# Kernel optimization log

Measured on AMD Instinct MI355X. Metric: run time of the kernel, lower is better.

## Reference

```python
import jax, jax.numpy as jnp
import numpy as np

N = 8192
DIM_IN = 1024
DIM_INNER = 1024
DIM_OUT = 1024


def setup_inputs() -> dict:
    key = jax.random.key(0)
    k1, k2, k3, k4 = jax.random.split(key, 4)
    x = jax.random.normal(k1, (N, DIM_IN), dtype=jnp.float32)
    # torch nn.Linear weights, stored transposed for right-multiplication
    Wqkv = jax.random.normal(k2, (DIM_IN, 3 * DIM_INNER), dtype=jnp.float32) * (DIM_IN ** -0.5)
    Wout = jax.random.normal(k3, (DIM_INNER, DIM_OUT), dtype=jnp.float32) * (DIM_INNER ** -0.5)
    bout = jax.random.normal(k4, (DIM_OUT,), dtype=jnp.float32) * 0.01
    return {"x": x, "Wqkv": Wqkv, "Wout": Wout, "bout": bout}


def reference(x, Wqkv, Wout, bout):
    scale = DIM_INNER ** -0.5
    qkv = x @ Wqkv                      # [N, 3*Di]
    q, k, v = jnp.split(qkv, 3, axis=-1)  # each [N, Di]
    sim = jnp.einsum('id,jd->ij', q, k) * scale  # [N, N]
    # causal mask: future positions (j > i) filled with -finfo.max
    i = jnp.arange(sim.shape[0])[:, None]
    j = jnp.arange(sim.shape[1])[None, :]
    sim = jnp.where(j > i, -jnp.finfo(sim.dtype).max, sim)
    attn = jax.nn.softmax(sim, axis=-1)
    out = jnp.einsum('ij,jd->id', attn, v)  # [N, Di]
    return out @ Wout + bout            # [N, Do]
```

## Files before the change

kernel.cpp:

```cpp
#include <hip/hip_runtime.h>
#include <hip/hip_bf16.h>


typedef __bf16 v8bf __attribute__((ext_vector_type(8)));
typedef float  v4f  __attribute__((ext_vector_type(4)));

struct __align__(8) S4 { short x, y, z, w; };

__device__ inline short f2bf(float f) {
  __hip_bfloat16 h = __float2bfloat16(f);
  return *reinterpret_cast<short*>(&h);
}
__device__ inline float bf2f(short s) {
  unsigned u = ((unsigned)(unsigned short)s) << 16;
  float f;
  __builtin_memcpy(&f, &u, 4);
  return f;
}

__device__ inline void stage_tile(const short* gbase, int ldg, short* lds, int tid) {
#pragma unroll
  for (int p = 0; p < 2; ++p) {
    const int c = p * 256 + tid;
    const int pos = (c & 3) ^ ((c >> 3) & 3);
    const short* g = gbase + (size_t)(c >> 2) * ldg + pos * 8;
    short* l = lds + p * 2048 + (tid >> 6) * 512;
    __builtin_amdgcn_global_load_lds(
        (__attribute__((address_space(1))) void*)(void*)g,
        (__attribute__((address_space(3))) void*)l, 16, 0, 0);
  }
}

__device__ inline void mma_step(const short* As, const short* Bs, v4f acc[4][4],
                                int lane, int wm, int wn) {
  const int qd = lane >> 4, r16 = lane & 15;
  const int sw = (qd ^ ((r16 >> 1) & 3)) * 8;
  const short* ab = As + (wm * 64 + r16) * 32 + sw;
  const short* bb = Bs + (wn * 64 + r16) * 32 + sw;
  v8bf a[4], b[4];
#pragma unroll
  for (int t = 0; t < 4; ++t) {
    a[t] = *(const v8bf*)(ab + t * 512);
    b[t] = *(const v8bf*)(bb + t * 512);
  }
#pragma unroll
  for (int mt = 0; mt < 4; ++mt)
#pragma unroll
    for (int nt = 0; nt < 4; ++nt)
      acc[mt][nt] = __builtin_amdgcn_mfma_f32_16x16x32_bf16(a[mt], b[nt], acc[mt][nt], 0, 0, 0);
}

#define ACC_INIT(acc)                              \
  _Pragma("unroll") for (int i_ = 0; i_ < 4; ++i_) \
  _Pragma("unroll") for (int j_ = 0; j_ < 4; ++j_) \
      acc[i_][j_] = (v4f){0.f, 0.f, 0.f, 0.f};

__global__ __launch_bounds__(256) void k_zerof(float* __restrict__ p, int n) {
  const int i = blockIdx.x * 256 + threadIdx.x;
  if (i < n) p[i] = 0.f;
}

__global__ __launch_bounds__(256) void k_detect(const unsigned short* __restrict__ xs,
                                                int* __restrict__ flag) {
  __shared__ int cnt;
  if (threadIdx.x == 0) cnt = 0;
  __syncthreads();
  int local = 0;
  for (int i = threadIdx.x; i < 4096; i += 256) {
    const unsigned e = (xs[i] >> 7) & 0xFFu;
    if (e >= 0xC0u) ++local;
  }
  if (local) atomicAdd(&cnt, local);
  __syncthreads();
  if (threadIdx.x == 0) *flag = (cnt > 8) ? 1 : 0;
}

__global__ __launch_bounds__(256) void k_convert(const void* __restrict__ in,
                                                 short* __restrict__ out, int n,
                                                 const int* __restrict__ flag) {
  const int stride = gridDim.x * blockDim.x;
  int i = blockIdx.x * blockDim.x + threadIdx.x;
  if (*flag != 0) {
    const float* p = (const float*)in;
    for (; i < n; i += stride) out[i] = f2bf(p[i]);
  } else {
    const short* p = (const short*)in;
    for (; i < n; i += stride) out[i] = p[i];
  }
}

__global__ __launch_bounds__(256) void k_to_f32(const void* __restrict__ in,
                                                float* __restrict__ out, int n,
                                                const int* __restrict__ flag) {
  const int stride = gridDim.x * blockDim.x;
  int i = blockIdx.x * blockDim.x + threadIdx.x;
  if (*flag != 0) {
    const float* p = (const float*)in;
    for (; i < n; i += stride) out[i] = p[i];
  } else {
    const short* p = (const short*)in;
    for (; i < n; i += stride) out[i] = bf2f(p[i]);
  }
}

__global__ __launch_bounds__(256) void k_convT(const void* __restrict__ in,
                                               short* __restrict__ out, int R, int C,
                                               const int* __restrict__ flag) {
  __shared__ short t[32][33];
  const int xx = threadIdx.x & 31, y0 = threadIdx.x >> 5;
  const int c0 = blockIdx.x * 32, r0 = blockIdx.y * 32;
  if (*flag != 0) {
    const float* p = (const float*)in;
#pragma unroll
    for (int i = 0; i < 4; ++i) {
      int r = y0 + i * 8;
      t[r][xx] = f2bf(p[(size_t)(r0 + r) * C + c0 + xx]);
    }
  } else {
    const short* p = (const short*)in;
#pragma unroll
    for (int i = 0; i < 4; ++i) {
      int r = y0 + i * 8;
      t[r][xx] = p[(size_t)(r0 + r) * C + c0 + xx];
    }
  }
  __syncthreads();
#pragma unroll
  for (int i = 0; i < 4; ++i) {
    int r = y0 + i * 8;
    out[(size_t)(c0 + r) * R + r0 + xx] = t[xx][r];
  }
}

__global__ __launch_bounds__(256) void k_gemm_qkv(const short* __restrict__ x,
                                                  const short* __restrict__ wt,
                                                  short* __restrict__ qk,
                                                  short* __restrict__ vT) {
  __shared__ short As[4096], Bs[4096];
  const int tid = threadIdx.x, lane = tid & 63, wave = tid >> 6;
  const int wm = wave >> 1, wn = wave & 1;
  const int m0 = blockIdx.x * 128, n0 = blockIdx.y * 128;
  v4f acc[4][4];
  ACC_INIT(acc)
  for (int k0 = 0; k0 < 1024; k0 += 32) {
    __syncthreads();
    stage_tile(x + (size_t)m0 * 1024 + k0, 1024, As, tid);
    stage_tile(wt + (size_t)n0 * 1024 + k0, 1024, Bs, tid);
    __syncthreads();
    mma_step(As, Bs, acc, lane, wm, wn);
  }
  const int qd = lane >> 4, c16 = lane & 15;
#pragma unroll
  for (int mt = 0; mt < 4; ++mt) {
    const int rl = wm * 64 + mt * 16 + qd * 4;
#pragma unroll
    for (int nt = 0; nt < 4; ++nt) {
      const int cl = wn * 64 + nt * 16 + c16;
      const int n = n0 + cl;
      if (n < 2048) {
#pragma unroll
        for (int r = 0; r < 4; ++r)
          qk[(size_t)(m0 + rl + r) * 2048 + n] = f2bf(acc[mt][nt][r]);
      } else {
        S4 p;
        p.x = f2bf(acc[mt][nt][0]);
        p.y = f2bf(acc[mt][nt][1]);
        p.z = f2bf(acc[mt][nt][2]);
        p.w = f2bf(acc[mt][nt][3]);
        *reinterpret_cast<S4*>(vT + (size_t)(n - 2048) * 8192 + (m0 + rl)) = p;
      }
    }
  }
}

__global__ __launch_bounds__(256) void k_qk_exp(const short* __restrict__ qk,
                                                short* __restrict__ E,
                                                float* __restrict__ l) {
  __shared__ short As[4096], Bs[4096];
  __shared__ float srow[128][2];
  const int tid = threadIdx.x, lane = tid & 63, wave = tid >> 6;
  const int wm = wave >> 1, wn = wave & 1;
  const int b = (int)blockIdx.x;
  int I = (int)((sqrtf(8.f * (float)b + 1.f) - 1.f) * 0.5f);
  while ((I + 1) * (I + 2) / 2 <= b) ++I;
  while (I * (I + 1) / 2 > b) --I;
  const int J = b - I * (I + 1) / 2;
  const int m0 = I * 128, n0 = J * 128;
  v4f acc[4][4];
  ACC_INIT(acc)
  for (int k0 = 0; k0 < 1024; k0 += 32) {
    __syncthreads();
    stage_tile(qk + (size_t)m0 * 2048 + k0, 2048, As, tid);
    stage_tile(qk + 1024 + (size_t)n0 * 2048 + k0, 2048, Bs, tid);
    __syncthreads();
    mma_step(As, Bs, acc, lane, wm, wn);
  }
  short* tb = E + (size_t)(I * (I + 1) / 2 + J) * 16384;
  const int qd = lane >> 4, c16 = lane & 15;
  float rp[4][4];
#pragma unroll
  for (int mt = 0; mt < 4; ++mt)
#pragma unroll
    for (int r = 0; r < 4; ++r) rp[mt][r] = 0.f;
#pragma unroll
  for (int mt = 0; mt < 4; ++mt) {
    const int rl = wm * 64 + mt * 16 + qd * 4;
#pragma unroll
    for (int nt = 0; nt < 4; ++nt) {
      const int cl = wn * 64 + nt * 16 + c16;
      const int gj = n0 + cl;
#pragma unroll
      for (int r = 0; r < 4; ++r) {
        const int gi = m0 + rl + r;
        const float s = fminf(acc[mt][nt][r] * 0.03125f, 60.f);
        const float e = (gj > gi) ? 0.f : __expf(s);
        tb[(rl + r) * 128 + cl] = f2bf(e);
        rp[mt][r] += e;
      }
    }
  }
#pragma unroll
  for (int mt = 0; mt < 4; ++mt)
#pragma unroll
    for (int r = 0; r < 4; ++r) {
      float v = rp[mt][r];
      v += __shfl_xor(v, 1);
      v += __shfl_xor(v, 2);
      v += __shfl_xor(v, 4);
      v += __shfl_xor(v, 8);
      rp[mt][r] = v;
    }
  if ((lane & 15) == 0) {
#pragma unroll
    for (int mt = 0; mt < 4; ++mt)
#pragma unroll
      for (int r = 0; r < 4; ++r)
        srow[wm * 64 + mt * 16 + qd * 4 + r][wn] = rp[mt][r];
  }
  __syncthreads();
  if (tid < 128) atomicAdd(&l[m0 + tid], srow[tid][0] + srow[tid][1]);
}

#define AS_ST 4112
#define BS_ST 2064
__device__ inline void pv_load(const short* __restrict__ Et, const short* __restrict__ vb,
                               v8bf av[8], v8bf bv[4], int tid) {
#pragma unroll
  for (int p = 0; p < 8; ++p) {
    const int c = p * 256 + tid;
    av[p] = *(const v8bf*)(Et + (c >> 4) * 128 + (c & 15) * 8);
  }
#pragma unroll
  for (int p = 0; p < 4; ++p) {
    const int c = p * 256 + tid;
    bv[p] = *(const v8bf*)(vb + (size_t)(c >> 4) * 8192 + (c & 15) * 8);
  }
}
__device__ inline void pv_write(short* __restrict__ As, short* __restrict__ Bs,
                                const v8bf av[8], const v8bf bv[4], int tid) {
#pragma unroll
  for (int p = 0; p < 8; ++p) {
    const int c = p * 256 + tid, cc = c & 15;
    const int pos = (cc & 3) ^ ((c >> 5) & 3);
    *(v8bf*)(As + (cc >> 2) * AS_ST + (c >> 4) * 32 + pos * 8) = av[p];
  }
#pragma unroll
  for (int p = 0; p < 4; ++p) {
    const int c = p * 256 + tid, cc = c & 15;
    const int pos = (cc & 3) ^ ((c >> 5) & 3);
    *(v8bf*)(Bs + (cc >> 2) * BS_ST + (c >> 4) * 32 + pos * 8) = bv[p];
  }
}

__global__ __launch_bounds__(256) void k_pv(const short* __restrict__ E,
                                            const short* __restrict__ vT,
                                            const float* __restrict__ l,
                                            short* __restrict__ attn) {
  __shared__ short As[4 * AS_ST];
  __shared__ short Bs[4 * BS_ST];
  const int tid = threadIdx.x, lane = tid & 63, wave = tid >> 6;
  const int wm = wave >> 1, wn = wave & 1;
  const int bx = (int)blockIdx.x;
  const int n0 = (int)blockIdx.y * 64;
  const int qd = lane >> 4, r16 = lane & 15;
  const int sw = (qd ^ ((r16 >> 1) & 3)) * 8;
  for (int half = 0; half < 2; ++half) {
    const int I = half ? 63 - bx : bx;
    const int m0 = I * 128;
    const short* Erow = E + (size_t)(I * (I + 1) / 2) * 16384;
    const short* vb = vT + (size_t)n0 * 8192;
    v4f acc[4][2];
#pragma unroll
    for (int mt = 0; mt < 4; ++mt)
#pragma unroll
      for (int nt = 0; nt < 2; ++nt) acc[mt][nt] = (v4f){0.f, 0.f, 0.f, 0.f};
    v8bf av[8], bv[4];
    pv_load(Erow, vb, av, bv, tid);
    __syncthreads();
    pv_write(As, Bs, av, bv, tid);
    __syncthreads();
    for (int J = 0; J <= I; ++J) {
      const bool more = (J < I);
      if (more) pv_load(Erow + (size_t)(J + 1) * 16384, vb + (J + 1) * 128, av, bv, tid);
#pragma unroll
      for (int jj = 0; jj < 4; ++jj) {
        const short* ab = As + jj * AS_ST + (wm * 64 + r16) * 32 + sw;
        const short* bb = Bs + jj * BS_ST + (wn * 32 + r16) * 32 + sw;
        v8bf a[4], b[2];
#pragma unroll
        for (int u = 0; u < 4; ++u) a[u] = *(const v8bf*)(ab + u * 512);
#pragma unroll
        for (int u = 0; u < 2; ++u) b[u] = *(const v8bf*)(bb + u * 512);
#pragma unroll
        for (int mt = 0; mt < 4; ++mt)
#pragma unroll
          for (int nt = 0; nt < 2; ++nt)
            acc[mt][nt] = __builtin_amdgcn_mfma_f32_16x16x32_bf16(a[mt], b[nt], acc[mt][nt], 0, 0, 0);
      }
      if (more) {
        __syncthreads();
        pv_write(As, Bs, av, bv, tid);
        __syncthreads();
      }
    }
    const int c16 = lane & 15;
#pragma unroll
    for (int mt = 0; mt < 4; ++mt) {
      const int rl = wm * 64 + mt * 16 + qd * 4;
      float inv[4];
#pragma unroll
      for (int r = 0; r < 4; ++r) inv[r] = 1.0f / fmaxf(l[m0 + rl + r], 1e-30f);
#pragma unroll
      for (int nt = 0; nt < 2; ++nt) {
        const int cl = wn * 32 + nt * 16 + c16;
#pragma unroll
        for (int r = 0; r < 4; ++r)
          attn[(size_t)(m0 + rl + r) * 1024 + n0 + cl] = f2bf(acc[mt][nt][r] * inv[r]);
      }
    }
  }
}

__global__ __launch_bounds__(256) void k_gemm_out(const short* __restrict__ attn,
                                                  const short* __restrict__ wt,
                                                  const float* __restrict__ bout,
                                                  float* __restrict__ out) {
  __shared__ short As[4096], Bs[4096];
  const int tid = threadIdx.x, lane = tid & 63, wave = tid >> 6;
  const int wm = wave >> 1, wn = wave & 1;
  const int m0 = blockIdx.x * 128, n0 = blockIdx.y * 128;
  v4f acc[4][4];
  ACC_INIT(acc)
  for (int k0 = 0; k0 < 1024; k0 += 32) {
    __syncthreads();
    stage_tile(attn + (size_t)m0 * 1024 + k0, 1024, As, tid);
    stage_tile(wt + (size_t)n0 * 1024 + k0, 1024, Bs, tid);
    __syncthreads();
    mma_step(As, Bs, acc, lane, wm, wn);
  }
  const int qd = lane >> 4, c16 = lane & 15;
#pragma unroll
  for (int mt = 0; mt < 4; ++mt) {
    const int rl = wm * 64 + mt * 16 + qd * 4;
#pragma unroll
    for (int nt = 0; nt < 4; ++nt) {
      const int cl = wn * 64 + nt * 16 + c16;
      const float bias = bout[n0 + cl];
#pragma unroll
      for (int r = 0; r < 4; ++r)
        out[(size_t)(m0 + rl + r) * 1024 + n0 + cl] = acc[mt][nt][r] + bias;
    }
  }
}

extern "C" void kernel_launch(void* const* d_in, const int* in_sizes, int n_in,
                              void* d_out, int out_size, void* d_ws, size_t ws_size,
                              hipStream_t stream) {
  (void)out_size; (void)ws_size;
  const void *x = d_in[0], *Wqkv = d_in[1], *Wout = d_in[2], *bout = d_in[3];
  for (int i = 0; i < n_in; ++i) {
    switch (in_sizes[i]) {
      case 8192 * 1024: x = d_in[i]; break;
      case 1024 * 3072: Wqkv = d_in[i]; break;
      case 1024 * 1024: Wout = d_in[i]; break;
      case 1024:        bout = d_in[i]; break;
      default: break;
    }
  }

  char* ws = (char*)d_ws;
  short* qk    = (short*)(ws);
  short* vT    = (short*)(ws + 33554432);
  short* E     = (short*)(ws + 50331648);
  short* xb    = (short*)(ws + 118489088);
  short* attn  = xb;
  short* WqT   = (short*)(ws + 135266304);
  short* WoT   = (short*)(ws + 141557760);
  float* boutf = (float*)(ws + 143654912);
  float* lsum  = (float*)(ws + 143659008);
  int*   flag  = (int*)  (ws + 143691776);

  k_detect<<<1, 256, 0, stream>>>((const unsigned short*)x, flag);
  k_zerof<<<32, 256, 0, stream>>>(lsum, 8192);
  k_convert<<<1024, 256, 0, stream>>>(x, xb, 8192 * 1024, flag);
  k_to_f32<<<1, 256, 0, stream>>>(bout, boutf, 1024, flag);
  k_convT<<<dim3(96, 32), 256, 0, stream>>>(Wqkv, WqT, 1024, 3072, flag);
  k_convT<<<dim3(32, 32), 256, 0, stream>>>(Wout, WoT, 1024, 1024, flag);
  k_gemm_qkv<<<dim3(64, 24), 256, 0, stream>>>(xb, WqT, qk, vT);
  k_qk_exp<<<dim3(2080), 256, 0, stream>>>(qk, E, lsum);
  k_pv<<<dim3(32, 16), 256, 0, stream>>>(E, vT, lsum, attn);
  k_gemm_out<<<dim3(64, 8), 256, 0, stream>>>(attn, WoT, boutf, (float*)d_out);
}
```

Before: 403.5 us.

## Store exp tiles in MFMA fragment layout and double-buffer V via direct LDS loads

The QK kernel now writes the exponentiated score tiles in the exact per-lane MFMA A-fragment order. This lets the PV kernel load A operands straight from global memory into registers and skip the LDS round-trip. V tiles are staged with global_load_lds into two swizzled LDS buffers, ping-ponged with one barrier per step instead of two. The aim is less LDS traffic and fewer syncs in the PV loop, at the cost of more registers (32 v8bf A fragments) and scattered 2-byte stores in the QK epilogue.

```diff
diff --git a/kernel.cpp b/kernel.cpp
--- a/kernel.cpp
+++ b/kernel.cpp
@@ -209,12 +209,14 @@
     for (int nt = 0; nt < 4; ++nt) {
       const int cl = wn * 64 + nt * 16 + c16;
       const int gj = n0 + cl;
+      const int jj = cl >> 5, qdc = (cl >> 3) & 3, jl = cl & 7;
+      short* dst = tb + (((wm * 4 + jj) * 4 + mt) * 512) + qdc * 128 + jl;
 #pragma unroll
       for (int r = 0; r < 4; ++r) {
         const int gi = m0 + rl + r;
         const float s = fminf(acc[mt][nt][r] * 0.03125f, 60.f);
         const float e = (gj > gi) ? 0.f : __expf(s);
-        tb[(rl + r) * 128 + cl] = f2bf(e);
+        dst[(qd * 4 + r) * 8] = f2bf(e);
         rp[mt][r] += e;
       }
     }
@@ -241,34 +243,41 @@
   if (tid < 128) atomicAdd(&l[m0 + tid], srow[tid][0] + srow[tid][1]);
 }
 
-#define AS_ST 4112
-#define BS_ST 2064
-__device__ inline void pv_load(const short* __restrict__ Et, const short* __restrict__ vb,
-                               v8bf av[8], v8bf bv[4], int tid) {
-#pragma unroll
-  for (int p = 0; p < 8; ++p) {
-    const int c = p * 256 + tid;
-    av[p] = *(const v8bf*)(Et + (c >> 4) * 128 + (c & 15) * 8);
-  }
+__device__ __forceinline__ void pv_loadA(v8bf a[16], const short* __restrict__ Et,
+                                         int wm16, int lane) {
+#pragma unroll
+  for (int t = 0; t < 16; ++t)
+    a[t] = *(const v8bf*)(Et + (size_t)(wm16 + t) * 512 + lane * 8);
+}
+
+__device__ __forceinline__ void pv_stageV(const short* __restrict__ vbJ,
+                                          short* __restrict__ lds, int tid) {
 #pragma unroll
   for (int p = 0; p < 4; ++p) {
     const int c = p * 256 + tid;
-    bv[p] = *(const v8bf*)(vb + (size_t)(c >> 4) * 8192 + (c & 15) * 8);
-  }
-}
-__device__ inline void pv_write(short* __restrict__ As, short* __restrict__ Bs,
-                                const v8bf av[8], const v8bf bv[4], int tid) {
-#pragma unroll
-  for (int p = 0; p < 8; ++p) {
-    const int c = p * 256 + tid, cc = c & 15;
-    const int pos = (cc & 3) ^ ((c >> 5) & 3);
-    *(v8bf*)(As + (cc >> 2) * AS_ST + (c >> 4) * 32 + pos * 8) = av[p];
-  }
-#pragma unroll
-  for (int p = 0; p < 4; ++p) {
-    const int c = p * 256 + tid, cc = c & 15;
-    const int pos = (cc & 3) ^ ((c >> 5) & 3);
-    *(v8bf*)(Bs + (cc >> 2) * BS_ST + (c >> 4) * 32 + pos * 8) = bv[p];
+    const int row = c >> 4;
+    const int gc = (c & 15) ^ (row & 15);
+    const short* g = vbJ + (size_t)row * 8192 + gc * 8;
+    short* lp = lds + (p * 256 + (tid >> 6) * 64) * 8;
+    __builtin_amdgcn_global_load_lds(
+        (__attribute__((address_space(1))) void*)(void*)g,
+        (__attribute__((address_space(3))) void*)lp, 16, 0, 0);
+  }
+}
+
+__device__ __forceinline__ void pv_compute(const v8bf a[16], const short* __restrict__ Vbuf,
+                                           v4f acc[4][2], int wn, int qd, int r16) {
+#pragma unroll
+  for (int jj = 0; jj < 4; ++jj) {
+    v8bf b[2];
+#pragma unroll
+    for (int u = 0; u < 2; ++u)
+      b[u] = *(const v8bf*)(Vbuf + (wn * 32 + u * 16 + r16) * 128 + (((jj * 4 + qd) ^ r16) * 8));
+#pragma unroll
+    for (int mt = 0; mt < 4; ++mt)
+#pragma unroll
+      for (int nt = 0; nt < 2; ++nt)
+        acc[mt][nt] = __builtin_amdgcn_mfma_f32_16x16x32_bf16(a[jj * 4 + mt], b[nt], acc[mt][nt], 0, 0, 0);
   }
 }
 
@@ -276,52 +285,42 @@
                                             const short* __restrict__ vT,
                                             const float* __restrict__ l,
                                             short* __restrict__ attn) {
-  __shared__ short As[4 * AS_ST];
-  __shared__ short Bs[4 * BS_ST];
+  __shared__ short Vb[2][8192];
   const int tid = threadIdx.x, lane = tid & 63, wave = tid >> 6;
   const int wm = wave >> 1, wn = wave & 1;
   const int bx = (int)blockIdx.x;
   const int n0 = (int)blockIdx.y * 64;
   const int qd = lane >> 4, r16 = lane & 15;
-  const int sw = (qd ^ ((r16 >> 1) & 3)) * 8;
+  const short* vb = vT + (size_t)n0 * 8192;
   for (int half = 0; half < 2; ++half) {
     const int I = half ? 63 - bx : bx;
     const int m0 = I * 128;
     const short* Erow = E + (size_t)(I * (I + 1) / 2) * 16384;
-    const short* vb = vT + (size_t)n0 * 8192;
     v4f acc[4][2];
 #pragma unroll
     for (int mt = 0; mt < 4; ++mt)
 #pragma unroll
       for (int nt = 0; nt < 2; ++nt) acc[mt][nt] = (v4f){0.f, 0.f, 0.f, 0.f};
-    v8bf av[8], bv[4];
-    pv_load(Erow, vb, av, bv, tid);
-    __syncthreads();
-    pv_write(As, Bs, av, bv, tid);
-    __syncthreads();
-    for (int J = 0; J <= I; ++J) {
-      const bool more = (J < I);
-      if (more) pv_load(Erow + (size_t)(J + 1) * 16384, vb + (J + 1) * 128, av, bv, tid);
-#pragma unroll
-      for (int jj = 0; jj < 4; ++jj) {
-        const short* ab = As + jj * AS_ST + (wm * 64 + r16) * 32 + sw;
-        const short* bb = Bs + jj * BS_ST + (wn * 32 + r16) * 32 + sw;
-        v8bf a[4], b[2];
-#pragma unroll
-        for (int u = 0; u < 4; ++u) a[u] = *(const v8bf*)(ab + u * 512);
-#pragma unroll
-        for (int u = 0; u < 2; ++u) b[u] = *(const v8bf*)(bb + u * 512);
-#pragma unroll
-        for (int mt = 0; mt < 4; ++mt)
-#pragma unroll
-          for (int nt = 0; nt < 2; ++nt)
-            acc[mt][nt] = __builtin_amdgcn_mfma_f32_16x16x32_bf16(a[mt], b[nt], acc[mt][nt], 0, 0, 0);
+    v8bf aA[16], aB[16];
+    __syncthreads();
+    pv_stageV(vb, Vb[0], tid);
+    pv_loadA(aA, Erow, wm * 16, lane);
+    __syncthreads();
+    for (int J = 0;; J += 2) {
+      if (J + 1 <= I) {
+        pv_loadA(aB, Erow + (size_t)(J + 1) * 16384, wm * 16, lane);
+        pv_stageV(vb + (J + 1) * 128, Vb[1], tid);
       }
-      if (more) {
-        __syncthreads();
-        pv_write(As, Bs, av, bv, tid);
-        __syncthreads();
+      pv_compute(aA, Vb[0], acc, wn, qd, r16);
+      if (J + 1 > I) break;
+      __syncthreads();
+      if (J + 2 <= I) {
+        pv_loadA(aA, Erow + (size_t)(J + 2) * 16384, wm * 16, lane);
+        pv_stageV(vb + (J + 2) * 128, Vb[0], tid);
       }
+      pv_compute(aB, Vb[1], acc, wn, qd, r16);
+      if (J + 2 > I) break;
+      __syncthreads();
     }
     const int c16 = lane & 15;
 #pragma unroll
```

Result: slower. 414.9 us (+2.8%).
